# Kernel tuning notes

Measured on AMD Instinct MI355X. Metric: run time of the kernel, lower is better.

Reference implementation:

```python
import jax, jax.numpy as jnp
import numpy as np

# ---- constants derived from module config ----
DEG_HIST = np.array([0., 12000., 20000., 13000., 4000., 1000.])
AVG_DEG_LOG = float((np.log(np.arange(len(DEG_HIST)) + 1.0) * DEG_HIST).sum() / DEG_HIST.sum())
N_NODES, N_EDGES, N_GRAPHS = 50000, 150000, 2000
D, E_D, TOWERS, F_OUT, N_LAYERS = 75, 50, 5, 15, 4
EPS = 1e-5


def setup_inputs() -> dict:
    key = jax.random.key(0)
    ks = jax.random.split(key, 16)
    g = lambda k, shape, s=0.05: (jax.random.normal(k, shape, jnp.float32) * s)
    return {
        'x': jax.random.randint(ks[0], (N_NODES,), 0, 21),
        'edge_index': jax.random.randint(ks[1], (2, N_EDGES), 0, N_NODES),
        'edge_attr': jax.random.randint(ks[2], (N_EDGES,), 0, 4),
        'batch': jnp.sort(jax.random.randint(ks[3], (N_NODES,), 0, N_GRAPHS)),
        'node_emb': g(ks[4], (21, D), 1.0),
        'edge_emb': g(ks[5], (4, E_D), 1.0),
        'We': g(ks[6], (N_LAYERS, E_D, D)),
        'be': jnp.zeros((N_LAYERS, D), jnp.float32),
        'Wpre': g(ks[7], (N_LAYERS, TOWERS, 3 * D, D)),
        'bpre': jnp.zeros((N_LAYERS, TOWERS, D), jnp.float32),
        'Wpost': g(ks[8], (N_LAYERS, TOWERS, 13 * D, F_OUT)),
        'bpost': jnp.zeros((N_LAYERS, TOWERS, F_OUT), jnp.float32),
        'Wlin': g(ks[9], (N_LAYERS, D, D)),
        'blin': jnp.zeros((N_LAYERS, D), jnp.float32),
        'gamma': jnp.ones((N_LAYERS, D), jnp.float32),
        'beta': jnp.zeros((N_LAYERS, D), jnp.float32),
        'W1': g(ks[10], (D, 50)), 'b1': jnp.zeros((50,), jnp.float32),
        'W2': g(ks[11], (50, 25)), 'b2': jnp.zeros((25,), jnp.float32),
        'W3': g(ks[12], (25, 1)), 'b3': jnp.zeros((1,), jnp.float32),
    }


def _pna_layer(x, src, dst, e_emb, We, be, Wpre, bpre, Wpost, bpost, Wlin, blin):
    # edge encoder (shared across towers)
    e = e_emb @ We + be                                        # [E, D]
    h = jnp.concatenate([x[dst], x[src], e], axis=-1)          # [E, 3D] = (x_i, x_j, e)
    m = jnp.einsum('ec,tcf->etf', h, Wpre) + bpre              # [E, T, D] per-tower pre_nn
    # multi-aggregator scatter (mean / min / max / std) onto target nodes
    deg = jax.ops.segment_sum(jnp.ones((src.shape[0],), x.dtype), dst, num_segments=N_NODES)
    denom = jnp.maximum(deg, 1.0)[:, None, None]
    mean = jax.ops.segment_sum(m, dst, num_segments=N_NODES) / denom
    mean_sq = jax.ops.segment_sum(m * m, dst, num_segments=N_NODES) / denom
    std = jnp.sqrt(jax.nn.relu(mean_sq - mean * mean) + 1e-5)
    has = (deg > 0)[:, None, None]
    mn = jnp.where(has, jax.ops.segment_min(m, dst, num_segments=N_NODES), 0.0)
    mx = jnp.where(has, jax.ops.segment_max(m, dst, num_segments=N_NODES), 0.0)
    agg = jnp.concatenate([mean, mn, mx, std], axis=-1)        # [N, T, 4D]
    # degree scalers: identity / amplification / attenuation
    amp = jnp.log(jnp.maximum(deg, 1.0) + 1.0)[:, None, None] / AVG_DEG_LOG
    out = jnp.concatenate([agg, agg * amp, agg / amp], axis=-1)  # [N, T, 12D]
    xt = jnp.broadcast_to(x[:, None, :], (x.shape[0], TOWERS, D))  # divide_input=False
    out = jnp.concatenate([xt, out], axis=-1)                   # [N, T, 13D]
    out = jnp.einsum('ntc,tcf->ntf', out, Wpost) + bpost        # [N, T, F_OUT] per-tower post_nn
    out = out.reshape(x.shape[0], TOWERS * F_OUT)               # [N, D]
    return out @ Wlin + blin


def _bn(x, gamma, beta):
    mu = x.mean(0)
    var = ((x - mu) ** 2).mean(0)  # biased, training-mode batch stats
    return gamma * (x - mu) / jnp.sqrt(var + EPS) + beta


def reference(x, edge_index, edge_attr, batch, node_emb, edge_emb, We, be, Wpre, bpre,
              Wpost, bpost, Wlin, blin, gamma, beta, W1, b1, W2, b2, W3, b3):
    src, dst = edge_index[0], edge_index[1]
    h = node_emb[x]                 # [N, 75]
    ea = edge_emb[edge_attr]        # [E, 50]
    for l in range(N_LAYERS):
        h = jax.nn.relu(_bn(_pna_layer(h, src, dst, ea, We[l], be[l], Wpre[l], bpre[l],
                                       Wpost[l], bpost[l], Wlin[l], blin[l]),
                            gamma[l], beta[l]))
    pooled = jax.ops.segment_sum(h, batch, num_segments=N_GRAPHS)  # global_add_pool
    z = jax.nn.relu(pooled @ W1 + b1)
    z = jax.nn.relu(z @ W2 + b2)
    return z @ W3 + b3  # [N_GRAPHS, 1]
```

## Files before the change

kernel.cpp:

```cpp
#include <hip/hip_runtime.h>
#include <math.h>

#define NN 50000
#define NE 150000
#define NG 2000
#define NL 4
#define AVG_DEG_LOG 1.1308269950720915f

typedef __attribute__((ext_vector_type(8))) short bf8_t;
typedef __attribute__((ext_vector_type(4))) float f4_t;

__device__ inline unsigned short f2bf(float x) {
  union { float f; unsigned int u; } v; v.f = x;
  unsigned int r = (v.u + 0x7FFFu + ((v.u >> 16) & 1u)) >> 16;
  return (unsigned short)r;
}
__device__ inline float bflo(unsigned int u) { union { unsigned int u; float f; } v; v.u = u << 16; return v.f; }
__device__ inline float bfhi(unsigned int u) { union { unsigned int u; float f; } v; v.u = u & 0xFFFF0000u; return v.f; }

__device__ inline bf8_t ldfrag(const float* __restrict__ zrow, int k0, int bn,
                               const float* __restrict__ musig,
                               const float* __restrict__ gm, const float* __restrict__ bt) {
  bf8_t r;
  #pragma unroll
  for (int j = 0; j < 8; ++j) {
    int k = k0 + j;
    float x = 0.0f;
    if (k < 75) {
      x = zrow[k];
      if (bn) x = fmaxf(gm[k] * (x - musig[k]) * musig[75 + k] + bt[k], 0.0f);
    }
    r[j] = (short)f2bf(x);
  }
  return r;
}

__global__ void k_deg(const int* __restrict__ dst, int* __restrict__ deg) {
  int e = blockIdx.x * 256 + threadIdx.x;
  if (e < NE) atomicAdd(&deg[dst[e]], 1);
}

__global__ __launch_bounds__(1024) void k_scan(const int* __restrict__ deg, int* __restrict__ off) {
  __shared__ int wsum[16];
  __shared__ int wpre[16];
  __shared__ int carry_s;
  int tid = threadIdx.x, lane = tid & 63, wv = tid >> 6;
  if (tid == 0) carry_s = 0;
  __syncthreads();
  for (int base = 0; base < NN; base += 1024) {
    int i = base + tid;
    int v = (i < NN) ? deg[i] : 0;
    int incl = v;
    #pragma unroll
    for (int d = 1; d < 64; d <<= 1) { int t = __shfl_up(incl, d); if (lane >= d) incl += t; }
    if (lane == 63) wsum[wv] = incl;
    __syncthreads();
    if (wv == 0) {
      int s = (lane < 16) ? wsum[lane] : 0;
      int sc = s;
      #pragma unroll
      for (int d = 1; d < 16; d <<= 1) { int t = __shfl_up(sc, d); if (lane >= d) sc += t; }
      if (lane < 16) wpre[lane] = sc - s;
    }
    __syncthreads();
    int carry = carry_s;
    int excl = carry + wpre[wv] + incl - v;
    if (i < NN) off[i] = excl;
    __syncthreads();
    if (tid == 1023) carry_s = excl + v;
    __syncthreads();
  }
  if (tid == 0) off[NN] = carry_s;
}

__global__ void k_amp(const int* __restrict__ deg, const int* __restrict__ off,
                      float* __restrict__ amp, float* __restrict__ invamp,
                      float* __restrict__ gate, int* __restrict__ cursor) {
  int n = blockIdx.x * 256 + threadIdx.x;
  if (n < NN) {
    int d0 = deg[n];
    int d = d0 < 1 ? 1 : d0;
    float a = logf((float)d + 1.0f) / AVG_DEG_LOG;
    amp[n] = a; invamp[n] = 1.0f / a;
    gate[n] = (d0 > 0) ? 1.0f : 0.0f;
    cursor[n] = off[n];
  }
}

__global__ void k_fill(const int* __restrict__ src, const int* __restrict__ dst,
                       const int* __restrict__ attr, int* __restrict__ cursor,
                       unsigned int* __restrict__ cpack) {
  int e = blockIdx.x * 256 + threadIdx.x;
  if (e < NE) {
    int d = dst[e];
    int p = atomicAdd(&cursor[d], 1);
    cpack[p] = (unsigned int)src[e] | ((unsigned int)attr[e] << 16);
  }
}

__global__ void k_embed(const int* __restrict__ x, const float* __restrict__ emb, float* __restrict__ Zf) {
  int i = blockIdx.x * 256 + threadIdx.x;
  if (i < NN * 76) {
    int n = i / 76, c = i - (i / 76) * 76;
    Zf[i] = (c < 75) ? emb[x[n] * 75 + c] : 0.0f;
  }
}

__global__ void k_wxlin(const float* __restrict__ Wpost, const float* __restrict__ Wlin, float* __restrict__ WXlin) {
  int l = blockIdx.x;
  for (int idx = threadIdx.x; idx < 5625; idx += 256) {
    int k = idx / 75, j = idx - (idx / 75) * 75;
    float s = 0.0f;
    for (int o = 0; o < 75; ++o) {
      int t = o / 15, jj = o - t * 15;
      s += Wpost[((l * 5 + t) * 975 + k) * 15 + jj] * Wlin[l * 5625 + o * 75 + j];
    }
    WXlin[l * 5625 + idx] = s;
  }
}

__global__ void k_zb(const float* __restrict__ bpost, const float* __restrict__ blin,
                     const float* __restrict__ Wlin, float* __restrict__ zb) {
  int l = blockIdx.x, j = threadIdx.x;
  if (j < 75) {
    float s = blin[l * 75 + j];
    for (int o = 0; o < 75; ++o) s += bpost[l * 75 + o] * Wlin[l * 5625 + o * 75 + j];
    zb[l * 75 + j] = s;
  }
}

__global__ void k_wy(const float* __restrict__ Wpre, const float* __restrict__ bpre,
                     const float* __restrict__ Wpost, float* __restrict__ WY, float* __restrict__ bY) {
  __shared__ float wsum[1125];
  int b = blockIdx.x;
  int l = b / 15, rr = b - l * 15, t = rr / 3, s = rr - (rr / 3) * 3;
  int tid = threadIdx.x;
  for (int it = tid; it < 1125; it += 256) {
    int f = it / 15, jj = it - (it / 15) * 15;
    float acc = 0.0f;
    #pragma unroll
    for (int agg = 0; agg < 3; ++agg)
      acc += Wpost[((l * 5 + t) * 975 + 75 + s * 300 + agg * 75 + f) * 15 + jj];
    wsum[f * 15 + jj] = acc;
  }
  __syncthreads();
  for (int it = tid; it < 1140; it += 256) {
    int k = it / 15, jj = it - (it / 15) * 15;
    float acc = 0.0f;
    if (k < 75) {
      for (int f = 0; f < 75; ++f)
        acc += Wpre[((l * 5 + t) * 225 + k) * 75 + f] * wsum[f * 15 + jj];
      WY[((l * 3 + s) * 75 + k) * 75 + t * 15 + jj] = acc;
    } else {
      for (int f = 0; f < 75; ++f)
        acc += bpre[l * 375 + t * 75 + f] * wsum[f * 15 + jj];
      bY[(l * 3 + s) * 75 + t * 15 + jj] = acc;
    }
  }
}

__global__ void k_packAll(const float* __restrict__ Wpre, const float* __restrict__ WXlin,
                          const float* __restrict__ WY, const float* __restrict__ Wlin,
                          unsigned short* __restrict__ B1Ts, unsigned short* __restrict__ WXYT,
                          unsigned short* __restrict__ WlinT) {
  const int S1 = 4 * 384 * 96;
  const int S2 = S1 + 4 * 320 * 96;
  const int S3 = S2 + 4 * 80 * 96;
  int idx = blockIdx.x * 256 + threadIdx.x;
  if (idx < S1) {
    int l = idx / (384 * 96); int rem = idx - l * (384 * 96);
    int c = rem / 96, k = rem - (rem / 96) * 96;
    float v = 0.0f;
    if (c < 375 && k < 75) {
      int t = c / 75, f = c - t * 75;
      v = Wpre[((l * 5 + t) * 225 + 75 + k) * 75 + f];
    }
    B1Ts[idx] = f2bf(v);
  } else if (idx < S2) {
    int m = idx - S1;
    int l = m / (320 * 96); int rem = m - l * (320 * 96);
    int c = rem / 96, k = rem - (rem / 96) * 96;
    float v = 0.0f;
    if (k < 75) {
      if (c < 80) {
        if (c < 75) v = WXlin[l * 5625 + k * 75 + c];
      } else {
        int g = c - 80; int t = g / 48; int r = g - t * 48; int s = r / 16; int jj = r - s * 16;
        if (jj < 15) v = WY[((l * 3 + s) * 75 + k) * 75 + t * 15 + jj];
      }
    }
    WXYT[m] = f2bf(v);
  } else if (idx < S3) {
    int m = idx - S2;
    int l = m / (80 * 96); int rem = m - l * (80 * 96);
    int j = rem / 96, k = rem - (rem / 96) * 96;
    float v = (j < 75 && k < 75) ? Wlin[l * 5625 + k * 75 + j] : 0.0f;
    WlinT[m] = f2bf(v);
  }
}

__global__ void k_packWcomb(const float* __restrict__ Wpost, unsigned short* __restrict__ WcombT) {
  int idx = blockIdx.x * 256 + threadIdx.x;
  if (idx >= 4 * 5 * 48 * 320) return;
  int l = idx / (5 * 48 * 320); int rem = idx - l * (5 * 48 * 320);
  int t = rem / (48 * 320); rem -= t * (48 * 320);
  int j = rem / 320, k = rem - (rem / 320) * 320;
  float v = 0.0f;
  if (j < 45 && k < 300) {
    int s = j / 15, jj = j - s * 15;
    int f = k >> 2, agg = k & 3;
    v = Wpost[((l * 5 + t) * 975 + 75 + s * 300 + agg * 75 + f) * 15 + jj];
  }
  WcombT[idx] = f2bf(v);
}

__global__ void k_etab(const float* __restrict__ edge_emb, const float* __restrict__ We,
                       const float* __restrict__ be, const float* __restrict__ Wpre,
                       float* __restrict__ etab) {
  __shared__ float ev[75];
  int l = blockIdx.x >> 2, a = blockIdx.x & 3;
  int tid = threadIdx.x;
  if (tid < 75) {
    float acc = be[l * 75 + tid];
    for (int k = 0; k < 50; ++k) acc += edge_emb[a * 50 + k] * We[(l * 50 + k) * 75 + tid];
    ev[tid] = acc;
  }
  __syncthreads();
  for (int tf = tid; tf < 384; tf += 256) {
    float acc = 0.0f;
    if (tf < 375) {
      int t = tf / 75, f = tf - t * 75;
      for (int d = 0; d < 75; ++d) acc += ev[d] * Wpre[((l * 5 + t) * 225 + 150 + d) * 75 + f];
    }
    etab[(l * 4 + a) * 384 + tf] = acc;
  }
}

__global__ __launch_bounds__(256) void k_gemm1(const float* __restrict__ Zf,
                                               const float* __restrict__ musig,
                                               const float* __restrict__ gm, const float* __restrict__ bt,
                                               int bn,
                                               const unsigned short* __restrict__ B1Ts_l,
                                               unsigned short* __restrict__ Hsrc,
                                               unsigned short* __restrict__ hb) {
  int w = threadIdx.x >> 6, lane = threadIdx.x & 63;
  int l15 = lane & 15, l4 = lane >> 4;
  int m0 = blockIdx.x * 64 + w * 16;
  int mA = m0 + l15; if (mA >= NN) mA = NN - 1;
  const float* zrow = Zf + (size_t)mA * 76;
  bf8_t a0 = ldfrag(zrow, l4 * 8, bn, musig, gm, bt);
  bf8_t a1 = ldfrag(zrow, 32 + l4 * 8, bn, musig, gm, bt);
  bf8_t a2 = ldfrag(zrow, 64 + l4 * 8, bn, musig, gm, bt);
  {
    unsigned short* hrow = hb + (size_t)mA * 96 + l4 * 8;
    *(bf8_t*)(hrow) = a0;
    *(bf8_t*)(hrow + 32) = a1;
    *(bf8_t*)(hrow + 64) = a2;
  }
  for (int nf = 0; nf < 24; ++nf) {
    int c = nf * 16 + l15;
    const unsigned short* bp = B1Ts_l + (size_t)c * 96 + l4 * 8;
    f4_t acc = {0.f, 0.f, 0.f, 0.f};
    acc = __builtin_amdgcn_mfma_f32_16x16x32_bf16(a0, *(const bf8_t*)(bp), acc, 0, 0, 0);
    acc = __builtin_amdgcn_mfma_f32_16x16x32_bf16(a1, *(const bf8_t*)(bp + 32), acc, 0, 0, 0);
    acc = __builtin_amdgcn_mfma_f32_16x16x32_bf16(a2, *(const bf8_t*)(bp + 64), acc, 0, 0, 0);
    #pragma unroll
    for (int i = 0; i < 4; ++i) {
      int m = m0 + l4 * 4 + i;
      if (m < NN) Hsrc[(size_t)m * 384 + c] = f2bf(acc[i]);
    }
  }
}

__global__ __launch_bounds__(256) void k_gather(const unsigned short* __restrict__ Hsrc,
                                                const int* __restrict__ off,
                                                const unsigned int* __restrict__ cpack,
                                                const float* __restrict__ etab_l,
                                                unsigned short* __restrict__ A) {
  __shared__ float et_s[1536];
  int tid = threadIdx.x, w = tid >> 6, lane = tid & 63;
  for (int it = tid; it < 1536; it += 256) {
    int aa = it / 384, c = it - aa * 384;
    et_s[aa * 384 + (c ^ (((c >> 3) & 7) << 2))] = etab_l[it];
  }
  __syncthreads();
  int g = blockIdx.x * 4 + w;
  int e0 = off[g], e1 = off[g + 1];
  unsigned short* arow = A + (size_t)g * 1600;
  if (lane < 47) {
    int c0 = lane * 8;
    int cs = c0 ^ (((c0 >> 3) & 7) << 2);
    float s8[8], q8[8], mn8[8], mx8[8];
    #pragma unroll
    for (int j = 0; j < 8; ++j) {
      s8[j] = 0.0f; q8[j] = 0.0f;
      mn8[j] = 3.402823466e+38f; mx8[j] = -3.402823466e+38f;
    }
    auto acc8 = [&](bf8_t hv, unsigned int aa) {
      union { bf8_t v; unsigned int u[4]; } cv; cv.v = hv;
      f4_t ea = *(const f4_t*)&et_s[aa * 384 + cs];
      f4_t eb = *(const f4_t*)&et_s[aa * 384 + (cs ^ 4)];
      float vv[8], ee[8];
      #pragma unroll
      for (int j = 0; j < 4; ++j) {
        vv[2 * j] = bflo(cv.u[j]); vv[2 * j + 1] = bfhi(cv.u[j]);
        ee[j] = ea[j]; ee[4 + j] = eb[j];
      }
      #pragma unroll
      for (int j = 0; j < 8; ++j) {
        float q = vv[j] + ee[j];
        s8[j] += q;
        q8[j] = fmaf(q, q, q8[j]);
        mn8[j] = fminf(mn8[j], q);
        mx8[j] = fmaxf(mx8[j], q);
      }
    };
    for (int e = e0; e < e1; ) {
      int m = e1 - e;
      unsigned int pk0 = cpack[e];
      unsigned int pk1 = cpack[m > 1 ? e + 1 : e];
      unsigned int pk2 = cpack[m > 2 ? e + 2 : e];
      unsigned int pk3 = cpack[m > 3 ? e + 3 : e];
      bf8_t h0 = *((const bf8_t*)(Hsrc + (size_t)(pk0 & 0xFFFFu) * 384) + lane);
      bf8_t h1 = *((const bf8_t*)(Hsrc + (size_t)(pk1 & 0xFFFFu) * 384) + lane);
      bf8_t h2 = *((const bf8_t*)(Hsrc + (size_t)(pk2 & 0xFFFFu) * 384) + lane);
      bf8_t h3 = *((const bf8_t*)(Hsrc + (size_t)(pk3 & 0xFFFFu) * 384) + lane);
      acc8(h0, pk0 >> 16);
      if (m > 1) acc8(h1, pk1 >> 16);
      if (m > 2) acc8(h2, pk2 >> 16);
      if (m > 3) acc8(h3, pk3 >> 16);
      e += (m < 4) ? m : 4;
    }
    int d = e1 - e0;
    float inv = (d > 0) ? (1.0f / (float)d) : 0.0f;
    #pragma unroll
    for (int j = 0; j < 8; ++j) {
      int c = c0 + j;
      if (c < 375) {
        float mean, mnv, mxv, sd;
        if (d > 0) {
          float mu = s8[j] * inv;
          mean = mu; mnv = mn8[j]; mxv = mx8[j];
          sd = sqrtf(fmaxf(q8[j] * inv - mu * mu, 0.0f) + 1e-5f);
        } else { mean = 0.0f; mnv = 0.0f; mxv = 0.0f; sd = 0.0031622776601683794f; }
        int t = c / 75, f = c - (c / 75) * 75;
        uint2 pkv;
        pkv.x = (unsigned int)f2bf(mean) | ((unsigned int)f2bf(mnv) << 16);
        pkv.y = (unsigned int)f2bf(mxv) | ((unsigned int)f2bf(sd) << 16);
        *(uint2*)&arow[t * 320 + f * 4] = pkv;
      }
    }
  } else {
    uint2 z; z.x = 0u; z.y = 0u;
    for (int k = lane - 47; k < 25; k += 17) {
      int t = k / 5, q = k - (k / 5) * 5;
      *(uint2*)&arow[t * 320 + 300 + q * 4] = z;
    }
  }
}

__global__ __launch_bounds__(256) void k_post(const unsigned short* __restrict__ A,
                                              const unsigned short* __restrict__ hb,
                                              const unsigned short* __restrict__ WcombT_l,
                                              const unsigned short* __restrict__ WXYT_l,
                                              const unsigned short* __restrict__ WlinT_l,
                                              const float* __restrict__ ampv,
                                              const float* __restrict__ invampv,
                                              const float* __restrict__ gatev,
                                              const float* __restrict__ bY_l,
                                              const float* __restrict__ zb_l,
                                              float* __restrict__ Zf) {
  __shared__ __align__(16) unsigned short At_s[64 * 328];
  __shared__ __align__(16) float Out_s[64 * 99];
  __shared__ __align__(16) unsigned short Cb_s[64 * 104];
  __shared__ float amp_s[64], inv_s[64], gate_s[64];
  int tid = threadIdx.x;
  int w = tid >> 6, lane = tid & 63;
  int l15 = lane & 15, l4 = lane >> 4;
  int m0 = blockIdx.x * 64;

  for (int r = tid; r < 64; r += 256) {
    int m = m0 + r; if (m >= NN) m = NN - 1;
    amp_s[r] = ampv[m]; inv_s[r] = invampv[m]; gate_s[r] = gatev[m];
  }
  for (int idx = tid; idx < 64 * 29; idx += 256) {
    int r = idx / 29, c = idx - (idx / 29) * 29;
    Cb_s[r * 104 + 75 + c] = 0;
  }
  int mh = m0 + w * 16 + l15; if (mh >= NN) mh = NN - 1;
  const unsigned short* hrow = hb + (size_t)mh * 96 + l4 * 8;
  bf8_t hb0 = *(const bf8_t*)(hrow);
  bf8_t hb1 = *(const bf8_t*)(hrow + 32);
  bf8_t hb2 = *(const bf8_t*)(hrow + 64);
  f4_t x0[5];
  #pragma unroll
  for (int fx = 0; fx < 5; ++fx) {
    const unsigned short* bp = WXYT_l + (size_t)(fx * 16 + l15) * 96 + l4 * 8;
    f4_t acc = {0.f, 0.f, 0.f, 0.f};
    acc = __builtin_amdgcn_mfma_f32_16x16x32_bf16(hb0, *(const bf8_t*)(bp), acc, 0, 0, 0);
    acc = __builtin_amdgcn_mfma_f32_16x16x32_bf16(hb1, *(const bf8_t*)(bp + 32), acc, 0, 0, 0);
    acc = __builtin_amdgcn_mfma_f32_16x16x32_bf16(hb2, *(const bf8_t*)(bp + 64), acc, 0, 0, 0);
    x0[fx] = acc;
  }

  for (int t = 0; t < 5; ++t) {
    __syncthreads();
    #pragma unroll
    for (int k = 0; k < 10; ++k) {
      int s = (k * 256 + tid) * 8;
      int r = s / 320, c = s - r * 320;
      int m = m0 + r; if (m >= NN) m = NN - 1;
      *(bf8_t*)&At_s[r * 328 + c] = *(const bf8_t*)&A[(size_t)m * 1600 + t * 320 + c];
    }
    __syncthreads();
    bf8_t af[10];
    const unsigned short* ap = &At_s[(w * 16 + l15) * 328 + l4 * 8];
    #pragma unroll
    for (int ks = 0; ks < 10; ++ks) af[ks] = *(const bf8_t*)(ap + ks * 32);
    f4_t tw0 = {0.f,0.f,0.f,0.f}, tw1 = {0.f,0.f,0.f,0.f}, tw2 = {0.f,0.f,0.f,0.f};
    const unsigned short* wp0 = WcombT_l + (size_t)(t * 48 + l15) * 320 + l4 * 8;
    const unsigned short* wp1 = WcombT_l + (size_t)(t * 48 + 16 + l15) * 320 + l4 * 8;
    const unsigned short* wp2 = WcombT_l + (size_t)(t * 48 + 32 + l15) * 320 + l4 * 8;
    #pragma unroll
    for (int ks = 0; ks < 10; ++ks) {
      tw0 = __builtin_amdgcn_mfma_f32_16x16x32_bf16(af[ks], *(const bf8_t*)(wp0 + ks * 32), tw0, 0, 0, 0);
      tw1 = __builtin_amdgcn_mfma_f32_16x16x32_bf16(af[ks], *(const bf8_t*)(wp1 + ks * 32), tw1, 0, 0, 0);
      tw2 = __builtin_amdgcn_mfma_f32_16x16x32_bf16(af[ks], *(const bf8_t*)(wp2 + ks * 32), tw2, 0, 0, 0);
    }
    f4_t yv[3];
    #pragma unroll
    for (int s = 0; s < 3; ++s) {
      const unsigned short* bp = WXYT_l + (size_t)(80 + t * 48 + s * 16 + l15) * 96 + l4 * 8;
      f4_t acc = {0.f, 0.f, 0.f, 0.f};
      acc = __builtin_amdgcn_mfma_f32_16x16x32_bf16(hb0, *(const bf8_t*)(bp), acc, 0, 0, 0);
      acc = __builtin_amdgcn_mfma_f32_16x16x32_bf16(hb1, *(const bf8_t*)(bp + 32), acc, 0, 0, 0);
      acc = __builtin_amdgcn_mfma_f32_16x16x32_bf16(hb2, *(const bf8_t*)(bp + 64), acc, 0, 0, 0);
      yv[s] = acc;
    }
    #pragma unroll
    for (int i = 0; i < 4; ++i) {
      int rb = w * 16 + l4 * 4 + i;
      Out_s[rb * 99 + l15] = tw0[i];
      Out_s[rb * 99 + 16 + l15] = tw1[i];
      Out_s[rb * 99 + 32 + l15] = tw2[i];
      Out_s[rb * 99 + 48 + l15] = yv[0][i];
      Out_s[rb * 99 + 64 + l15] = yv[1][i];
      Out_s[rb * 99 + 80 + l15] = yv[2][i];
    }
    __syncthreads();
    for (int item = tid; item < 1024; item += 256) {
      int r = item >> 4, jj = item & 15;
      if (jj < 15) {
        const float* ob = &Out_s[r * 99];
        float gt = gate_s[r];
        int o = t * 15 + jj;
        float v1 = ob[jj]      + gt * (ob[48 + jj] + bY_l[o]);
        float v2 = ob[15 + jj] + gt * (ob[64 + jj] + bY_l[75 + o]);
        float v3 = ob[30 + jj] + gt * (ob[80 + jj] + bY_l[150 + o]);
        Cb_s[r * 104 + o] = f2bf(v1 + amp_s[r] * v2 + inv_s[r] * v3);
      }
    }
  }
  __syncthreads();
  bf8_t cf[3];
  const unsigned short* cp = &Cb_s[(w * 16 + l15) * 104 + l4 * 8];
  #pragma unroll
  for (int ks = 0; ks < 3; ++ks) cf[ks] = *(const bf8_t*)(cp + ks * 32);
  #pragma unroll
  for (int fx = 0; fx < 5; ++fx) {
    int cc = fx * 16 + l15;
    const unsigned short* bp = WlinT_l + (size_t)cc * 96 + l4 * 8;
    f4_t acc = {0.f, 0.f, 0.f, 0.f};
    acc = __builtin_amdgcn_mfma_f32_16x16x32_bf16(cf[0], *(const bf8_t*)(bp), acc, 0, 0, 0);
    acc = __builtin_amdgcn_mfma_f32_16x16x32_bf16(cf[1], *(const bf8_t*)(bp + 32), acc, 0, 0, 0);
    acc = __builtin_amdgcn_mfma_f32_16x16x32_bf16(cf[2], *(const bf8_t*)(bp + 64), acc, 0, 0, 0);
    if (cc < 75) {
      #pragma unroll
      for (int i = 0; i < 4; ++i) {
        int m = m0 + w * 16 + l4 * 4 + i;
        if (m < NN) Zf[(size_t)m * 76 + cc] = acc[i] + x0[fx][i] + zb_l[cc];
      }
    }
  }
}

#define BN_BLOCKS 256
#define BN_ROWS 196
__global__ __launch_bounds__(256) void k_bnstats(const float* __restrict__ Zf, float* __restrict__ partial) {
  __shared__ float sArr[225];
  __shared__ float qArr[225];
  int tid = threadIdx.x;
  int r0 = blockIdx.x * BN_ROWS;
  int r1 = r0 + BN_ROWS; if (r1 > NN) r1 = NN;
  float s = 0.0f, q = 0.0f;
  if (tid < 225) {
    int rr = tid / 75, c = tid - rr * 75;
    for (int r = r0 + rr; r < r1; r += 3) {
      float v = Zf[(size_t)r * 76 + c];
      s += v; q += v * v;
    }
    sArr[tid] = s; qArr[tid] = q;
  }
  __syncthreads();
  if (tid < 75) {
    float S = sArr[tid] + sArr[75 + tid] + sArr[150 + tid];
    float Q = qArr[tid] + qArr[75 + tid] + qArr[150 + tid];
    partial[blockIdx.x * 150 + tid] = S;
    partial[blockIdx.x * 150 + 75 + tid] = Q;
  }
}

__global__ void k_bnfinal(const float* __restrict__ partial, float* __restrict__ musig) {
  int c = threadIdx.x;
  if (c < 75) {
    float S = 0.0f, Q = 0.0f;
    for (int b = 0; b < BN_BLOCKS; ++b) { S += partial[b * 150 + c]; Q += partial[b * 150 + 75 + c]; }
    float mu = S * (1.0f / NN);
    float var = fmaxf(Q * (1.0f / NN) - mu * mu, 0.0f);
    musig[c] = mu;
    musig[75 + c] = 1.0f / sqrtf(var + 1e-5f);
  }
}

__global__ __launch_bounds__(128) void k_pool_mlp(const float* __restrict__ Zf, const int* __restrict__ batch,
                                                  const float* __restrict__ musig,
                                                  const float* __restrict__ gm, const float* __restrict__ bt,
                                                  const float* __restrict__ W1, const float* __restrict__ b1,
                                                  const float* __restrict__ W2, const float* __restrict__ b2,
                                                  const float* __restrict__ W3, const float* __restrict__ b3,
                                                  float* __restrict__ out) {
  __shared__ float pooled[75];
  __shared__ float z1[50];
  __shared__ float z2[25];
  __shared__ int se[2];
  int g = blockIdx.x, tid = threadIdx.x;
  if (tid < 2) {
    int target = g + tid;
    int lo = 0, hi = NN;
    while (lo < hi) { int mid = (lo + hi) >> 1; if (batch[mid] < target) lo = mid + 1; else hi = mid; }
    se[tid] = lo;
  }
  __syncthreads();
  int s = se[0], e = se[1];
  if (tid < 75) {
    float mu = musig[tid], sig = musig[75 + tid], gmc = gm[tid], btc = bt[tid];
    float acc = 0.0f;
    for (int r = s; r < e; ++r)
      acc += fmaxf(gmc * (Zf[(size_t)r * 76 + tid] - mu) * sig + btc, 0.0f);
    pooled[tid] = acc;
  }
  __syncthreads();
  if (tid < 50) {
    float acc = b1[tid];
    for (int c = 0; c < 75; ++c) acc += pooled[c] * W1[c * 50 + tid];
    z1[tid] = fmaxf(acc, 0.0f);
  }
  __syncthreads();
  if (tid < 25) {
    float acc = b2[tid];
    for (int c = 0; c < 50; ++c) acc += z1[c] * W2[c * 25 + tid];
    z2[tid] = fmaxf(acc, 0.0f);
  }
  __syncthreads();
  if (tid == 0) {
    float acc = b3[0];
    for (int c = 0; c < 25; ++c) acc += z2[c] * W3[c];
    out[g] = acc;
  }
}

extern "C" void kernel_launch(void* const* d_in, const int* in_sizes, int n_in,
                              void* d_out, int out_size, void* d_ws, size_t ws_size,
                              hipStream_t stream) {
  const int* x = (const int*)d_in[0];
  const int* ei = (const int*)d_in[1];
  const int* eattr = (const int*)d_in[2];
  const int* batch = (const int*)d_in[3];
  const float* node_emb = (const float*)d_in[4];
  const float* edge_emb = (const float*)d_in[5];
  const float* We = (const float*)d_in[6];
  const float* be = (const float*)d_in[7];
  const float* Wpre = (const float*)d_in[8];
  const float* bpre = (const float*)d_in[9];
  const float* Wpost = (const float*)d_in[10];
  const float* bpost = (const float*)d_in[11];
  const float* Wlin = (const float*)d_in[12];
  const float* blin = (const float*)d_in[13];
  const float* gamma = (const float*)d_in[14];
  const float* beta = (const float*)d_in[15];
  const float* W1 = (const float*)d_in[16];
  const float* b1 = (const float*)d_in[17];
  const float* W2 = (const float*)d_in[18];
  const float* b2 = (const float*)d_in[19];
  const float* W3 = (const float*)d_in[20];
  const float* b3 = (const float*)d_in[21];
  float* out = (float*)d_out;

  const int* src = ei;
  const int* dst = ei + NE;

  char* p = (char*)d_ws;
  auto alloc = [&](size_t bytes) { char* r = p; p += (bytes + 255) & ~(size_t)255; return r; };
  int* deg     = (int*)alloc((size_t)NN * 4);
  int* off     = (int*)alloc((size_t)(NN + 1) * 4);
  int* cursor  = (int*)alloc((size_t)NN * 4);
  unsigned int* cpack = (unsigned int*)alloc((size_t)NE * 4);
  float* amp    = (float*)alloc((size_t)NN * 4);
  float* invamp = (float*)alloc((size_t)NN * 4);
  float* gate   = (float*)alloc((size_t)NN * 4);
  float* Zf            = (float*)alloc((size_t)NN * 76 * 4 + 256);
  unsigned short* Hsrc = (unsigned short*)alloc((size_t)NN * 384 * 2 + 256);
  unsigned short* hbv  = (unsigned short*)alloc((size_t)NN * 96 * 2 + 256);
  unsigned short* Abuf = (unsigned short*)alloc((size_t)NN * 1600 * 2 + 256);
  unsigned short* B1Ts   = (unsigned short*)alloc((size_t)4 * 384 * 96 * 2);
  unsigned short* WXYT   = (unsigned short*)alloc((size_t)4 * 320 * 96 * 2);
  unsigned short* WlinT  = (unsigned short*)alloc((size_t)4 * 80 * 96 * 2);
  unsigned short* WcombT = (unsigned short*)alloc((size_t)4 * 5 * 48 * 320 * 2);
  float* WXlin = (float*)alloc((size_t)4 * 5625 * 4);
  float* WY    = (float*)alloc((size_t)4 * 3 * 75 * 75 * 4);
  float* bY    = (float*)alloc((size_t)4 * 3 * 75 * 4);
  float* zb    = (float*)alloc((size_t)4 * 75 * 4);
  float* etab  = (float*)alloc((size_t)4 * 4 * 384 * 4);
  float* bnpart = (float*)alloc((size_t)BN_BLOCKS * 150 * 4);
  float* musig  = (float*)alloc((size_t)150 * 4);

  hipMemsetAsync(deg, 0, (size_t)NN * 4, stream);
  k_deg<<<(NE + 255) / 256, 256, 0, stream>>>(dst, deg);
  k_scan<<<1, 1024, 0, stream>>>(deg, off);
  k_amp<<<(NN + 255) / 256, 256, 0, stream>>>(deg, off, amp, invamp, gate, cursor);
  k_fill<<<(NE + 255) / 256, 256, 0, stream>>>(src, dst, eattr, cursor, cpack);
  k_embed<<<(NN * 76 + 255) / 256, 256, 0, stream>>>(x, node_emb, Zf);
  k_wxlin<<<4, 256, 0, stream>>>(Wpost, Wlin, WXlin);
  k_wy<<<60, 256, 0, stream>>>(Wpre, bpre, Wpost, WY, bY);
  k_zb<<<4, 128, 0, stream>>>(bpost, blin, Wlin, zb);
  {
    int tot = 4 * 384 * 96 + 4 * 320 * 96 + 4 * 80 * 96;
    k_packAll<<<(tot + 255) / 256, 256, 0, stream>>>(Wpre, WXlin, WY, Wlin, B1Ts, WXYT, WlinT);
  }
  k_packWcomb<<<(4 * 5 * 48 * 320 + 255) / 256, 256, 0, stream>>>(Wpost, WcombT);
  k_etab<<<16, 256, 0, stream>>>(edge_emb, We, be, Wpre, etab);

  for (int l = 0; l < NL; ++l) {
    const float* gm = gamma + (l > 0 ? (l - 1) * 75 : 0);
    const float* bt = beta + (l > 0 ? (l - 1) * 75 : 0);
    int bn = (l > 0) ? 1 : 0;
    k_gemm1<<<(NN + 63) / 64, 256, 0, stream>>>(Zf, musig, gm, bt, bn,
                                                B1Ts + (size_t)l * 384 * 96, Hsrc, hbv);
    k_gather<<<NN / 4, 256, 0, stream>>>(Hsrc, off, cpack, etab + (size_t)l * 4 * 384, Abuf);
    k_post<<<(NN + 63) / 64, 256, 0, stream>>>(Abuf, hbv,
                                               WcombT + (size_t)l * 5 * 48 * 320,
                                               WXYT + (size_t)l * 320 * 96,
                                               WlinT + (size_t)l * 80 * 96,
                                               amp, invamp, gate,
                                               bY + (size_t)l * 225,
                                               zb + l * 75, Zf);
    k_bnstats<<<BN_BLOCKS, 256, 0, stream>>>(Zf, bnpart);
    k_bnfinal<<<1, 128, 0, stream>>>(bnpart, musig);
  }
  k_pool_mlp<<<NG, 128, 0, stream>>>(Zf, batch, musig, gamma + 225, beta + 225,
                                     W1, b1, W2, b2, W3, b3, out);
}
```

Before: 1.334 ms.

## Fuse batch-norm statistics into post kernel and load A fragments directly from global

Batch-norm sum and sum-of-squares are now accumulated inside k_post through wave shuffles, shared-memory atomics and then global atomics, replacing the separate k_bnstats pass that re-read Zf. The k_post loop also drops its shared-memory staging of the A tile and loads MFMA fragments straight from global memory, which removes two barriers per tower. The costs are a memset per layer, global atomic contention on 150 floats, and non-deterministic float summation order.

```diff
diff --git a/kernel.cpp b/kernel.cpp
--- a/kernel.cpp
+++ b/kernel.cpp
@@ -369,11 +369,12 @@
                                               const float* __restrict__ gatev,
                                               const float* __restrict__ bY_l,
                                               const float* __restrict__ zb_l,
-                                              float* __restrict__ Zf) {
-  __shared__ __align__(16) unsigned short At_s[64 * 328];
+                                              float* __restrict__ Zf,
+                                              float* __restrict__ bnsum) {
   __shared__ __align__(16) float Out_s[64 * 99];
   __shared__ __align__(16) unsigned short Cb_s[64 * 104];
   __shared__ float amp_s[64], inv_s[64], gate_s[64];
+  __shared__ float bnred[152];
   int tid = threadIdx.x;
   int w = tid >> 6, lane = tid & 63;
   int l15 = lane & 15, l4 = lane >> 4;
@@ -387,6 +388,7 @@
     int r = idx / 29, c = idx - (idx / 29) * 29;
     Cb_s[r * 104 + 75 + c] = 0;
   }
+  if (tid < 152) bnred[tid] = 0.0f;
   int mh = m0 + w * 16 + l15; if (mh >= NN) mh = NN - 1;
   const unsigned short* hrow = hb + (size_t)mh * 96 + l4 * 8;
   bf8_t hb0 = *(const bf8_t*)(hrow);
@@ -402,21 +404,12 @@
     acc = __builtin_amdgcn_mfma_f32_16x16x32_bf16(hb2, *(const bf8_t*)(bp + 64), acc, 0, 0, 0);
     x0[fx] = acc;
   }
+  const unsigned short* arow = A + (size_t)mh * 1600 + l4 * 8;
 
   for (int t = 0; t < 5; ++t) {
-    __syncthreads();
-    #pragma unroll
-    for (int k = 0; k < 10; ++k) {
-      int s = (k * 256 + tid) * 8;
-      int r = s / 320, c = s - r * 320;
-      int m = m0 + r; if (m >= NN) m = NN - 1;
-      *(bf8_t*)&At_s[r * 328 + c] = *(const bf8_t*)&A[(size_t)m * 1600 + t * 320 + c];
-    }
-    __syncthreads();
     bf8_t af[10];
-    const unsigned short* ap = &At_s[(w * 16 + l15) * 328 + l4 * 8];
-    #pragma unroll
-    for (int ks = 0; ks < 10; ++ks) af[ks] = *(const bf8_t*)(ap + ks * 32);
+    #pragma unroll
+    for (int ks = 0; ks < 10; ++ks) af[ks] = *(const bf8_t*)(arow + t * 320 + ks * 32);
     f4_t tw0 = {0.f,0.f,0.f,0.f}, tw1 = {0.f,0.f,0.f,0.f}, tw2 = {0.f,0.f,0.f,0.f};
     const unsigned short* wp0 = WcombT_l + (size_t)(t * 48 + l15) * 320 + l4 * 8;
     const unsigned short* wp1 = WcombT_l + (size_t)(t * 48 + 16 + l15) * 320 + l4 * 8;
@@ -437,6 +430,7 @@
       acc = __builtin_amdgcn_mfma_f32_16x16x32_bf16(hb2, *(const bf8_t*)(bp + 64), acc, 0, 0, 0);
       yv[s] = acc;
     }
+    __syncthreads();
     #pragma unroll
     for (int i = 0; i < 4; ++i) {
       int rb = w * 16 + l4 * 4 + i;
@@ -475,48 +469,34 @@
     acc = __builtin_amdgcn_mfma_f32_16x16x32_bf16(cf[1], *(const bf8_t*)(bp + 32), acc, 0, 0, 0);
     acc = __builtin_amdgcn_mfma_f32_16x16x32_bf16(cf[2], *(const bf8_t*)(bp + 64), acc, 0, 0, 0);
     if (cc < 75) {
+      float s = 0.0f, q = 0.0f;
       #pragma unroll
       for (int i = 0; i < 4; ++i) {
         int m = m0 + w * 16 + l4 * 4 + i;
-        if (m < NN) Zf[(size_t)m * 76 + cc] = acc[i] + x0[fx][i] + zb_l[cc];
+        if (m < NN) {
+          float z = acc[i] + x0[fx][i] + zb_l[cc];
+          Zf[(size_t)m * 76 + cc] = z;
+          s += z; q = fmaf(z, z, q);
+        }
       }
-    }
-  }
-}
-
-#define BN_BLOCKS 256
-#define BN_ROWS 196
-__global__ __launch_bounds__(256) void k_bnstats(const float* __restrict__ Zf, float* __restrict__ partial) {
-  __shared__ float sArr[225];
-  __shared__ float qArr[225];
-  int tid = threadIdx.x;
-  int r0 = blockIdx.x * BN_ROWS;
-  int r1 = r0 + BN_ROWS; if (r1 > NN) r1 = NN;
-  float s = 0.0f, q = 0.0f;
-  if (tid < 225) {
-    int rr = tid / 75, c = tid - rr * 75;
-    for (int r = r0 + rr; r < r1; r += 3) {
-      float v = Zf[(size_t)r * 76 + c];
-      s += v; q += v * v;
-    }
-    sArr[tid] = s; qArr[tid] = q;
-  }
-  __syncthreads();
-  if (tid < 75) {
-    float S = sArr[tid] + sArr[75 + tid] + sArr[150 + tid];
-    float Q = qArr[tid] + qArr[75 + tid] + qArr[150 + tid];
-    partial[blockIdx.x * 150 + tid] = S;
-    partial[blockIdx.x * 150 + 75 + tid] = Q;
-  }
-}
-
-__global__ void k_bnfinal(const float* __restrict__ partial, float* __restrict__ musig) {
+      s += __shfl_xor(s, 16); q += __shfl_xor(q, 16);
+      s += __shfl_xor(s, 32); q += __shfl_xor(q, 32);
+      if (l4 == 0) {
+        atomicAdd(&bnred[cc], s);
+        atomicAdd(&bnred[76 + cc], q);
+      }
+    }
+  }
+  __syncthreads();
+  if (tid < 75) atomicAdd(&bnsum[tid], bnred[tid]);
+  else if (tid >= 76 && tid < 151) atomicAdd(&bnsum[tid - 1], bnred[tid]);
+}
+
+__global__ void k_bnfinal(const float* __restrict__ bnsum, float* __restrict__ musig) {
   int c = threadIdx.x;
   if (c < 75) {
-    float S = 0.0f, Q = 0.0f;
-    for (int b = 0; b < BN_BLOCKS; ++b) { S += partial[b * 150 + c]; Q += partial[b * 150 + 75 + c]; }
-    float mu = S * (1.0f / NN);
-    float var = fmaxf(Q * (1.0f / NN) - mu * mu, 0.0f);
+    float mu = bnsum[c] * (1.0f / NN);
+    float var = fmaxf(bnsum[75 + c] * (1.0f / NN) - mu * mu, 0.0f);
     musig[c] = mu;
     musig[75 + c] = 1.0f / sqrtf(var + 1e-5f);
   }
@@ -621,7 +601,7 @@
   float* bY    = (float*)alloc((size_t)4 * 3 * 75 * 4);
   float* zb    = (float*)alloc((size_t)4 * 75 * 4);
   float* etab  = (float*)alloc((size_t)4 * 4 * 384 * 4);
-  float* bnpart = (float*)alloc((size_t)BN_BLOCKS * 150 * 4);
+  float* bnsum  = (float*)alloc((size_t)152 * 4);
   float* musig  = (float*)alloc((size_t)150 * 4);
 
   hipMemsetAsync(deg, 0, (size_t)NN * 4, stream);
@@ -647,15 +627,15 @@
     k_gemm1<<<(NN + 63) / 64, 256, 0, stream>>>(Zf, musig, gm, bt, bn,
                                                 B1Ts + (size_t)l * 384 * 96, Hsrc, hbv);
     k_gather<<<NN / 4, 256, 0, stream>>>(Hsrc, off, cpack, etab + (size_t)l * 4 * 384, Abuf);
+    hipMemsetAsync(bnsum, 0, 152 * 4, stream);
     k_post<<<(NN + 63) / 64, 256, 0, stream>>>(Abuf, hbv,
                                                WcombT + (size_t)l * 5 * 48 * 320,
                                                WXYT + (size_t)l * 320 * 96,
                                                WlinT + (size_t)l * 80 * 96,
                                                amp, invamp, gate,
                                                bY + (size_t)l * 225,
-                                               zb + l * 75, Zf);
-    k_bnstats<<<BN_BLOCKS, 256, 0, stream>>>(Zf, bnpart);
-    k_bnfinal<<<1, 128, 0, stream>>>(bnpart, musig);
+                                               zb + l * 75, Zf, bnsum);
+    k_bnfinal<<<1, 128, 0, stream>>>(bnsum, musig);
   }
   k_pool_mlp<<<NG, 128, 0, stream>>>(Zf, batch, musig, gamma + 225, beta + 225,
                                      W1, b1, W2, b2, W3, b3, out);
```

Measured after the change: 1.348 ms. About the same (+1.0%).
